# Kernel optimization log

Hardware: AMD Instinct MI355X
Metric: run time of the kernel (lower is better)

Reference implementation:

```python
import jax, jax.numpy as jnp
import numpy as np
from jax import lax

DN = ('NHWC', 'HWIO', 'NHWC')


def conv_same(x, w):
    return lax.conv_general_dilated(x, w, window_strides=(1, 1), padding='SAME',
                                    dimension_numbers=DN)


def dwconv(x, w):
    # w: (kh, kw, F, 1) TF depthwise layout -> HWIO (kh, kw, 1, F), groups=F
    F = w.shape[2]
    return lax.conv_general_dilated(x, jnp.transpose(w, (0, 1, 3, 2)),
                                    window_strides=(1, 1), padding='SAME',
                                    dimension_numbers=DN, feature_group_count=F)


def hard_sigmoid(x):
    return jnp.clip(0.2 * x + 0.5, 0.0, 1.0)


def setup_inputs() -> dict:
    key = jax.random.key(0)
    ks = jax.random.split(key, 10)
    B, H, W, Cin, F = 16, 128, 128, 64, 64
    s = 0.05
    return {
        'inputs': jax.random.normal(ks[0], (B, H, W, Cin), jnp.float32),
        'h0': jax.random.normal(ks[1], (B, H, W, F), jnp.float32),
        'c0': jax.random.normal(ks[2], (B, H, W, F), jnp.float32),
        'm0': jax.random.normal(ks[3], (B, H, W, F), jnp.float32),
        'kernel': jax.random.normal(ks[4], (3, 3, Cin, 4 * F), jnp.float32) * s,
        'recurrent_kernel': jax.random.normal(ks[5], (3, 3, F, 4 * F), jnp.float32) * s,
        'bias': jnp.concatenate([jnp.zeros((F,), jnp.float32),
                                 jnp.ones((F,), jnp.float32),
                                 jnp.zeros((2 * F,), jnp.float32)]),
        'sa_kernel': jax.random.normal(ks[6], (1, 1, F, 5), jnp.float32) * s,
        'kernel_z': jax.random.normal(ks[7], (3, 3, 2, F), jnp.float32) * s,
        'depth_wise_kernel': jax.random.normal(ks[8], (3, 3, F, 6), jnp.float32) * s,
        'sa_bias': jnp.zeros((3 * F,), jnp.float32),
    }


def reference(inputs, h0, c0, m0, kernel, recurrent_kernel, bias, sa_kernel,
              kernel_z, depth_wise_kernel, sa_bias):
    F = h0.shape[-1]
    # --- ConvLSTM gates (no dropout: all four gates share the same input, so
    # a single fused conv over the 4F-channel kernel is the same math) ---
    xz = conv_same(inputs, kernel) + bias  # [B,H,W,4F]
    hz = conv_same(h0, recurrent_kernel)   # [B,H,W,4F]
    z = xz + hz
    zi_, zf_, zc_, zo_ = jnp.split(z, 4, axis=-1)
    i = hard_sigmoid(zi_)
    f = hard_sigmoid(zf_)
    c = f * c0 + i * jnp.tanh(zc_)
    o = hard_sigmoid(zo_)
    h = o * jnp.tanh(c)  # [B,H,W,F]

    # --- Self-attention memory (SAM) module; 1x1 convs -> channel contractions ---
    w = sa_kernel[0, 0]  # [F,5]
    v_h = jnp.einsum('bhwc,c->bhw', h, w[:, 0])
    k_h = jnp.einsum('bhwc,c->bhw', h, w[:, 1])
    q_h = jnp.einsum('bhwc,c->bhw', h, w[:, 2])
    k_m = jnp.einsum('bhwc,c->bhw', m0, w[:, 3])
    v_m = jnp.einsum('bhwc,c->bhw', m0, w[:, 4])

    alpha_m = jax.nn.softmax(jnp.matmul(q_h, k_m), axis=-1)  # [B,H,H] (H==W)
    alpha_h = jax.nn.softmax(jnp.matmul(q_h, k_h), axis=-1)
    z_m = jnp.matmul(alpha_m, v_m)  # [B,H,W]
    z_h = jnp.matmul(alpha_h, v_h)

    zi = conv_same(jnp.stack([z_h, z_m], axis=-1), kernel_z)  # [B,H,W,F]

    dw = depth_wise_kernel  # [3,3,F,6]
    b_i, b_g, b_o = jnp.split(sa_bias, 3)
    i2 = jax.nn.sigmoid(dwconv(zi, dw[..., 0:1]) + dwconv(h, dw[..., 1:2]) + b_i)
    g = jnp.tanh(dwconv(zi, dw[..., 2:3]) + dwconv(h, dw[..., 3:4]) + b_g)
    o2 = jax.nn.sigmoid(dwconv(zi, dw[..., 4:5]) + dwconv(h, dw[..., 5:6]) + b_o)

    m_t = (1.0 - i2) * m0 + i2 * g
    h_hat = m_t * o2
    return h_hat, c, m_t
```

## Files before the change

### kernel.cpp

```cpp
#include <hip/hip_runtime.h>

#define BB 16
#define HH 128
#define WW 128
#define FF 64
#define NPIX (BB*HH*WW)

typedef short bf16x8 __attribute__((ext_vector_type(8)));
typedef float f32x4 __attribute__((ext_vector_type(4)));

__device__ __forceinline__ float bf2f(unsigned int u){ return __uint_as_float(u<<16); }
__device__ __forceinline__ unsigned short f2bf(float f){
  unsigned u = __float_as_uint(f);
  u += 0x7fffu + ((u>>16)&1u);
  return (unsigned short)(u>>16);
}
__device__ __forceinline__ float hsig(float x){ return fminf(fmaxf(fmaf(0.2f,x,0.5f),0.f),1.f); }
__device__ __forceinline__ float tanh_fast(float x){
  float e = __expf(2.f*x);
  return 1.f - 2.f/(e + 1.f);
}
__device__ __forceinline__ void gload_lds16(const void* g, void* l){
  __builtin_amdgcn_global_load_lds(
      (const __attribute__((address_space(1))) unsigned int*)g,
      (__attribute__((address_space(3))) unsigned int*)l, 16, 0, 0);
}

__global__ __launch_bounds__(256) void prep_all(
    const float* __restrict__ in, const float* __restrict__ h0,
    const float* __restrict__ kern, const float* __restrict__ rkern,
    unsigned short* __restrict__ Xp, unsigned short* __restrict__ Wg){
  const int blk = blockIdx.x;
  const int t = threadIdx.x;
  if (blk < 33){
    int i = blk*256 + t;
    if (i >= 16*516) return;
    int b = i / 516, r = i % 516;
    int y, x;
    if (r < 130){ y = 0; x = r; }
    else if (r < 260){ y = 129; x = r-130; }
    else if (r < 388){ y = r-260+1; x = 0; }
    else { y = r-388+1; x = 129; }
    unsigned short* p = Xp + (((size_t)(b*130 + y)*130) + x)*128;
    uint4 z = {0u,0u,0u,0u};
    #pragma unroll
    for (int c=0;c<16;++c) ((uint4*)p)[c] = z;
  } else if (blk < 33 + 16384){
    int gi = (blk-33)*256 + t;
    int pix = gi >> 4;
    int ch8 = (gi & 15) * 8;
    const float* src = (ch8 < 64) ? (in + (size_t)pix*64 + ch8)
                                  : (h0 + (size_t)pix*64 + (ch8-64));
    float4 v0 = *(const float4*)src;
    float4 v1 = *(const float4*)(src+4);
    uint4 o;
    o.x = (unsigned)f2bf(v0.x) | ((unsigned)f2bf(v0.y)<<16);
    o.y = (unsigned)f2bf(v0.z) | ((unsigned)f2bf(v0.w)<<16);
    o.z = (unsigned)f2bf(v1.x) | ((unsigned)f2bf(v1.y)<<16);
    o.w = (unsigned)f2bf(v1.z) | ((unsigned)f2bf(v1.w)<<16);
    int b = pix >> 14, y = (pix >> 7) & 127, x = pix & 127;
    *(uint4*)(Xp + (((size_t)(b*130 + y+1)*130) + (x+1))*128 + ch8) = o;
  } else {
    int k = blk - (33 + 16384);
    int n = t;
    int tap = k >> 7, c = k & 127;
    float v = (c < 64) ? kern[((size_t)(tap*64 + c))*256 + n]
                       : rkern[((size_t)(tap*64 + (c-64)))*256 + n];
    Wg[(size_t)n*1152 + k] = f2bf(v);
  }
}

__global__ __launch_bounds__(256, 2) void gates_kernel(
    const unsigned short* __restrict__ Xp,
    const unsigned short* __restrict__ Wg,
    const float* __restrict__ bias,
    const float* __restrict__ c0,
    float* __restrict__ c_out,
    unsigned short* __restrict__ h_bf){
  __shared__ unsigned short As[2][130*128];
  const int gid = blockIdx.x;
  const int swz = (gid & 7)*256 + (gid >> 3);
  const int b  = swz >> 7;
  const int y  = swz & 127;
  const int tid = threadIdx.x;
  const int l = tid & 63;
  const int wid = tid >> 6;
  const int l15 = l & 15, l4 = l >> 4;
  const int n0 = wid*16 + l15;

  const unsigned short* brow[4];
  #pragma unroll
  for (int g=0; g<4; ++g) brow[g] = Wg + (size_t)(g*64 + n0)*1152 + l4*8;

  f32x4 acc[8][4];
  #pragma unroll
  for (int mf=0;mf<8;++mf)
    #pragma unroll
    for (int g=0;g<4;++g) acc[mf][g] = (f32x4){0.f,0.f,0.f,0.f};

  auto stage = [&](int buf, int dyi){
    const unsigned short* gbase = Xp + ((size_t)((b*130 + y + dyi)*130))*128;
    unsigned short* lbase = &As[buf][0];
    #pragma unroll
    for (int it=0; it<8; ++it){
      int q = it*256 + tid;
      int px = q >> 4, c = q & 15;
      int cs = c ^ (px & 7);
      gload_lds16(gbase + (size_t)px*128 + cs*8, lbase + (size_t)q*8);
    }
    if (l < 8){
      int q = 2048 + wid*8 + l;
      int px = q >> 4, c = q & 15;
      int cs = c ^ (px & 7);
      gload_lds16(gbase + (size_t)px*128 + cs*8, lbase + (size_t)q*8);
    }
  };

  stage(0, 0);
  for (int dyi = 0; dyi < 3; ++dyi){
    if (dyi < 2){
      stage((dyi+1)&1, dyi+1);
      asm volatile("s_waitcnt vmcnt(9)" ::: "memory");
    } else {
      asm volatile("s_waitcnt vmcnt(0)" ::: "memory");
    }
    __builtin_amdgcn_sched_barrier(0);
    __builtin_amdgcn_s_barrier();
    __builtin_amdgcn_sched_barrier(0);
    const unsigned short* asb = &As[dyi&1][0];
    #pragma unroll
    for (int dxi = 0; dxi < 3; ++dxi){
      const int tap = dyi*3 + dxi;
      #pragma unroll
      for (int ksc = 0; ksc < 2; ++ksc){
        bf16x8 bfr[4][2];
        #pragma unroll
        for (int g=0; g<4; ++g)
          #pragma unroll
          for (int k2=0; k2<2; ++k2)
            bfr[g][k2] = *(const bf16x8*)(brow[g] + tap*128 + (ksc*2+k2)*32);
        #pragma unroll
        for (int k2=0; k2<2; ++k2){
          const int cd = (ksc*2+k2)*4 + l4;
          #pragma unroll
          for (int mf=0; mf<8; ++mf){
            const int px = mf*16 + l15 + dxi;
            bf16x8 a = *(const bf16x8*)(asb + (size_t)px*128 + ((cd ^ (px & 7))*8));
            #pragma unroll
            for (int g=0;g<4;++g)
              acc[mf][g] = __builtin_amdgcn_mfma_f32_16x16x32_bf16(a, bfr[g][k2], acc[mf][g], 0,0,0);
          }
        }
      }
    }
    __builtin_amdgcn_sched_barrier(0);
    __builtin_amdgcn_s_barrier();
    __builtin_amdgcn_sched_barrier(0);
  }
  const float b0 = bias[n0], b1 = bias[64+n0], b2 = bias[128+n0], b3 = bias[192+n0];
  const size_t prow = (size_t)(b*128 + y)*128;
  #pragma unroll
  for (int mf=0;mf<8;++mf){
    #pragma unroll
    for (int r=0;r<4;++r){
      const int x = mf*16 + l4*4 + r;
      const size_t p = prow + x;
      const float zi_ = acc[mf][0][r] + b0;
      const float zf_ = acc[mf][1][r] + b1;
      const float zc_ = acc[mf][2][r] + b2;
      const float zo_ = acc[mf][3][r] + b3;
      const float iv = hsig(zi_), fv = hsig(zf_), ov = hsig(zo_);
      const float cv = fv*c0[p*64 + n0] + iv*tanh_fast(zc_);
      const float hv = ov*tanh_fast(cv);
      c_out[p*64 + n0] = cv;
      h_bf[p*64 + n0] = f2bf(hv);
    }
  }
}

__global__ __launch_bounds__(256) void qkv_kernel(
    const unsigned short* __restrict__ h_bf, const float* __restrict__ m0,
    const float* __restrict__ sak,
    float* __restrict__ q_h, float* __restrict__ k_h, float* __restrict__ v_h,
    float* __restrict__ k_m, float* __restrict__ v_m){
  __shared__ float wS[320];
  for (int i = threadIdx.x; i < 320; i += 256) wS[i] = sak[i];
  __syncthreads();
  const int p = blockIdx.x*256 + threadIdx.x;
  const unsigned short* hp = h_bf + (size_t)p*64;
  const float* mp = m0 + (size_t)p*64;
  float a0=0,a1=0,a2=0,a3=0,a4=0;
  #pragma unroll
  for (int ch = 0; ch < 64; ch += 8){
    uint4 hu = *(const uint4*)(hp + ch);
    float4 ma = *(const float4*)(mp + ch);
    float4 mb = *(const float4*)(mp + ch + 4);
    float hv[8] = { bf2f(hu.x&0xffffu), bf2f(hu.x>>16), bf2f(hu.y&0xffffu), bf2f(hu.y>>16),
                    bf2f(hu.z&0xffffu), bf2f(hu.z>>16), bf2f(hu.w&0xffffu), bf2f(hu.w>>16) };
    float mv[8] = { ma.x,ma.y,ma.z,ma.w, mb.x,mb.y,mb.z,mb.w };
    #pragma unroll
    for (int jj=0;jj<8;++jj){
      const float* w = &wS[(ch+jj)*5];
      a0 = fmaf(hv[jj], w[0], a0);
      a1 = fmaf(hv[jj], w[1], a1);
      a2 = fmaf(hv[jj], w[2], a2);
      a3 = fmaf(mv[jj], w[3], a3);
      a4 = fmaf(mv[jj], w[4], a4);
    }
  }
  v_h[p]=a0; k_h[p]=a1; q_h[p]=a2; k_m[p]=a3; v_m[p]=a4;
}

__global__ __launch_bounds__(256) void attn_kernel(
    const float* __restrict__ q_h, const float* __restrict__ k_h, const float* __restrict__ v_h,
    const float* __restrict__ k_m, const float* __restrict__ v_m,
    float* __restrict__ z_h, float* __restrict__ z_m){
  __shared__ float Kl[128][132];
  __shared__ float Vl[128][132];
  __shared__ float q2[8][132];
  __shared__ float al[8][132];
  const int bid = blockIdx.x;
  const int b = bid >> 4;
  const int type = (bid >> 3) & 1;
  const int rb = bid & 7;
  const float* K = (type ? k_m : k_h) + (size_t)b*16384;
  const float* V = (type ? v_m : v_h) + (size_t)b*16384;
  const float* Q = q_h + (size_t)b*16384;
  float* Z = (type ? z_m : z_h) + (size_t)b*16384;
  const int t = threadIdx.x;
  const int jq = t & 31;
  const int r8 = t >> 5;

  for (int base = 0; base < 16384; base += 1024){
    const int idx = base + t*4;
    const int w = idx >> 7, j = idx & 127;
    const float4 kv = *(const float4*)(K + idx);
    const float4 vv = *(const float4*)(V + idx);
    *(float4*)&Kl[w][j] = kv;
    *(float4*)&Vl[w][j] = vv;
  }

  for (int p = 0; p < 2; ++p){
    __syncthreads();
    for (int idx = t; idx < 1024; idx += 256)
      q2[idx>>7][idx&127] = Q[(rb*16 + p*8 + (idx>>7))*128 + (idx&127)];
    __syncthreads();
    const int i = rb*16 + p*8 + r8;
    float s0=0.f,s1=0.f,s2=0.f,s3=0.f;
    #pragma unroll 8
    for (int w=0; w<128; ++w){
      const float qv = q2[r8][w];
      const float4 kv = *(const float4*)&Kl[w][jq*4];
      s0 = fmaf(qv, kv.x, s0); s1 = fmaf(qv, kv.y, s1);
      s2 = fmaf(qv, kv.z, s2); s3 = fmaf(qv, kv.w, s3);
    }
    float mx = fmaxf(fmaxf(s0,s1), fmaxf(s2,s3));
    #pragma unroll
    for (int o=1;o<32;o<<=1) mx = fmaxf(mx, __shfl_xor(mx, o));
    const float p0 = __expf(s0-mx), p1 = __expf(s1-mx);
    const float p2 = __expf(s2-mx), p3 = __expf(s3-mx);
    float sm = (p0+p1)+(p2+p3);
    #pragma unroll
    for (int o=1;o<32;o<<=1) sm += __shfl_xor(sm, o);
    const float inv = 1.f/sm;
    *(float4*)&al[r8][jq*4] = make_float4(p0*inv, p1*inv, p2*inv, p3*inv);
    __syncthreads();
    float z0=0.f,z1=0.f,z2=0.f,z3=0.f;
    #pragma unroll 8
    for (int w=0; w<128; ++w){
      const float av = al[r8][w];
      const float4 vv = *(const float4*)&Vl[w][jq*4];
      z0 = fmaf(av, vv.x, z0); z1 = fmaf(av, vv.y, z1);
      z2 = fmaf(av, vv.z, z2); z3 = fmaf(av, vv.w, z3);
    }
    *(float4*)(Z + (size_t)i*128 + jq*4) = make_float4(z0,z1,z2,z3);
  }
}

__global__ __launch_bounds__(512) void final_fused(
    const float* __restrict__ z_h, const float* __restrict__ z_m,
    const float* __restrict__ kz,
    const unsigned short* __restrict__ h_bf,
    const float* __restrict__ m0, const float* __restrict__ dwk,
    const float* __restrict__ sab,
    float* __restrict__ hhat, float* __restrict__ m_t){
  __shared__ unsigned short zi[4][128][64];
  const int f = threadIdx.x & 63;
  const int g = threadIdx.x >> 6;
  const int blk = blockIdx.x;
  const int b = blk >> 6;
  const int y0 = (blk & 63) * 2;

  {
    const int ry = g >> 1;
    const int xh = g & 1;
    const int yy = y0 - 1 + ry;
    const int x0 = xh * 64;
    if ((unsigned)yy >= 128u){
      for (int i=0;i<64;++i) zi[ry][x0+i][f] = 0;
    } else {
      float w0[9], w1[9];
      #pragma unroll
      for (int tap=0; tap<9; ++tap){
        w0[tap] = kz[tap*128 + f];
        w1[tap] = kz[tap*128 + 64 + f];
      }
      const float* zhr = z_h + (size_t)(b*128 + yy)*128;
      const float* zmr = z_m + (size_t)(b*128 + yy)*128;
      const bool ym = (yy > 0), yp = (yy < 127);
      float az[3][3], am[3][3];
      auto ldc = [&](int x, float (&Z)[3], float (&M)[3]){
        if ((unsigned)x < 128u){
          Z[0] = ym ? zhr[x-128] : 0.f;  M[0] = ym ? zmr[x-128] : 0.f;
          Z[1] = zhr[x];                 M[1] = zmr[x];
          Z[2] = yp ? zhr[x+128] : 0.f;  M[2] = yp ? zmr[x+128] : 0.f;
        } else { Z[0]=Z[1]=Z[2]=0.f; M[0]=M[1]=M[2]=0.f; }
      };
      ldc(x0-1, az[0], am[0]);
      ldc(x0,   az[1], am[1]);
      for (int i=0; i<64; ++i){
        const int x = x0 + i;
        ldc(x+1, az[2], am[2]);
        float acc = 0.f;
        #pragma unroll
        for (int tap=0; tap<9; ++tap){
          const int dy = tap/3, dx = tap%3;
          acc = fmaf(az[dx][dy], w0[tap], acc);
          acc = fmaf(am[dx][dy], w1[tap], acc);
        }
        zi[ry][x][f] = f2bf(acc);
        #pragma unroll
        for (int k=0;k<3;++k){
          az[0][k]=az[1][k]; az[1][k]=az[2][k];
          am[0][k]=am[1][k]; am[1][k]=am[2][k];
        }
      }
    }
  }
  __syncthreads();

  const int r2 = g >> 2;
  const int xq = g & 3;
  const int y = y0 + r2;
  const size_t rb = (size_t)(b*128 + y)*128;
  float wv[9][6];
  #pragma unroll
  for (int tap=0;tap<9;++tap)
    #pragma unroll
    for (int jj=0;jj<6;++jj) wv[tap][jj] = dwk[(tap*64 + f)*6 + jj];
  const float bi = sab[f], bg = sab[64+f], bo = sab[128+f];
  const bool ym = (y > 0), yp = (y < 127);
  float vz[3][3], vh[3][3];
  auto ldc2 = [&](int x, float (&Z)[3], float (&H)[3]){
    if ((unsigned)x < 128u){
      const size_t base = (rb + x)*64 + f;
      H[0] = ym ? bf2f(h_bf[base - 8192]) : 0.f;
      H[1] = bf2f(h_bf[base]);
      H[2] = yp ? bf2f(h_bf[base + 8192]) : 0.f;
      Z[0] = bf2f(zi[r2  ][x][f]);
      Z[1] = bf2f(zi[r2+1][x][f]);
      Z[2] = bf2f(zi[r2+2][x][f]);
    } else { Z[0]=Z[1]=Z[2]=0.f; H[0]=H[1]=H[2]=0.f; }
  };
  const int x0 = xq*32;
  ldc2(x0-1, vz[0], vh[0]);
  ldc2(x0,   vz[1], vh[1]);
  for (int i=0; i<32; ++i){
    const int x = x0 + i;
    ldc2(x+1, vz[2], vh[2]);
    float si=0.f, sg=0.f, so=0.f;
    #pragma unroll
    for (int tap=0;tap<9;++tap){
      const int dy = tap/3, dx = tap%3;
      const float zv = vz[dx][dy], hv = vh[dx][dy];
      si = fmaf(zv, wv[tap][0], si); si = fmaf(hv, wv[tap][1], si);
      sg = fmaf(zv, wv[tap][2], sg); sg = fmaf(hv, wv[tap][3], sg);
      so = fmaf(zv, wv[tap][4], so); so = fmaf(hv, wv[tap][5], so);
    }
    const size_t p = rb + x;
    const float i2 = 1.f/(1.f+__expf(-(si+bi)));
    const float gg = tanh_fast(sg+bg);
    const float o2 = 1.f/(1.f+__expf(-(so+bo)));
    const float mv = m0[p*64+f];
    const float mt = (1.f-i2)*mv + i2*gg;
    hhat[p*64+f] = mt*o2;
    m_t[p*64+f]  = mt;
    #pragma unroll
    for (int k=0;k<3;++k){
      vz[0][k]=vz[1][k]; vz[1][k]=vz[2][k];
      vh[0][k]=vh[1][k]; vh[1][k]=vh[2][k];
    }
  }
}

extern "C" void kernel_launch(void* const* d_in, const int* in_sizes, int n_in,
                              void* d_out, int out_size, void* d_ws, size_t ws_size,
                              hipStream_t stream){
  const float* inputs = (const float*)d_in[0];
  const float* h0p    = (const float*)d_in[1];
  const float* c0p    = (const float*)d_in[2];
  const float* m0p    = (const float*)d_in[3];
  const float* kern   = (const float*)d_in[4];
  const float* rkern  = (const float*)d_in[5];
  const float* biasp  = (const float*)d_in[6];
  const float* sakp   = (const float*)d_in[7];
  const float* kzp    = (const float*)d_in[8];
  const float* dwkp   = (const float*)d_in[9];
  const float* sabp   = (const float*)d_in[10];
  float* out = (float*)d_out;
  char* ws = (char*)d_ws;

  constexpr size_t SZ_XP  = (size_t)16*130*130*128*2;
  constexpr size_t SZ_WG  = (size_t)256*1152*2;
  constexpr size_t SZ_HBF = (size_t)NPIX*64*2;
  constexpr size_t SZA    = (size_t)NPIX*4;
  constexpr size_t OFF_XP  = 0;
  constexpr size_t OFF_WG  = OFF_XP + SZ_XP;
  constexpr size_t OFF_HBF = OFF_WG + SZ_WG;
  constexpr size_t OFF_Q   = OFF_HBF + SZ_HBF;
  constexpr size_t OFF_KH  = OFF_Q  + SZA;
  constexpr size_t OFF_VH  = OFF_KH + SZA;
  constexpr size_t OFF_KM  = OFF_VH + SZA;
  constexpr size_t OFF_VM  = OFF_KM + SZA;
  constexpr size_t OFF_ZH  = OFF_VM + SZA;
  constexpr size_t OFF_ZM  = OFF_ZH + SZA;

  unsigned short* Xp  = (unsigned short*)(ws + OFF_XP);
  unsigned short* Wg  = (unsigned short*)(ws + OFF_WG);
  unsigned short* Hbf = (unsigned short*)(ws + OFF_HBF);
  float* Qh = (float*)(ws + OFF_Q);
  float* Kh = (float*)(ws + OFF_KH);
  float* Vh = (float*)(ws + OFF_VH);
  float* Km = (float*)(ws + OFF_KM);
  float* Vm = (float*)(ws + OFF_VM);
  float* Zh = (float*)(ws + OFF_ZH);
  float* Zm = (float*)(ws + OFF_ZM);

  prep_all<<<33 + 16384 + 1152, 256, 0, stream>>>(inputs, h0p, kern, rkern, Xp, Wg);
  gates_kernel<<<2048, 256, 0, stream>>>(Xp, Wg, biasp, c0p,
                                         out + (size_t)NPIX*64, Hbf);
  qkv_kernel<<<NPIX/256, 256, 0, stream>>>(Hbf, m0p, sakp, Qh, Kh, Vh, Km, Vm);
  attn_kernel<<<256, 256, 0, stream>>>(Qh, Kh, Vh, Km, Vm, Zh, Zm);
  final_fused<<<1024, 512, 0, stream>>>(Zh, Zm, kzp, Hbf, m0p, dwkp, sabp,
                                        out, out + 2*(size_t)NPIX*64);
}
```

Measured before the change: 401.8 us.

## Restructure gates conv GEMM to two-row tiles with LDS-staged weights

The gates kernel now processes two output rows per 512-thread block and iterates over 18 K-slices (tap × 64-channel half). Each slice double-buffers both activations and a permuted weight tile into LDS through async global-to-LDS loads, rather than reading weights from global memory inside the MFMA loop. Weights are reordered in prep so each wave's gate columns are contiguous. The change also adds intra-slice barriers and s_setprio around the MFMA bursts. It trades the old per-row activation reuse across dx taps for more barriers and a larger per-slice LDS footprint.

```diff
diff --git a/kernel.cpp b/kernel.cpp
--- a/kernel.cpp
+++ b/kernel.cpp
@@ -62,35 +62,38 @@
     *(uint4*)(Xp + (((size_t)(b*130 + y+1)*130) + (x+1))*128 + ch8) = o;
   } else {
     int k = blk - (33 + 16384);
-    int n = t;
+    int np = t;
     int tap = k >> 7, c = k & 127;
+    int wid = np >> 6, r = np & 63;
+    int gate = r >> 4, ch16 = r & 15;
+    int n = gate*64 + wid*16 + ch16;
     float v = (c < 64) ? kern[((size_t)(tap*64 + c))*256 + n]
                        : rkern[((size_t)(tap*64 + (c-64)))*256 + n];
-    Wg[(size_t)n*1152 + k] = f2bf(v);
-  }
-}
-
-__global__ __launch_bounds__(256, 2) void gates_kernel(
+    Wg[(size_t)np*1152 + k] = f2bf(v);
+  }
+}
+
+__global__ __launch_bounds__(512, 1) void gates_kernel(
     const unsigned short* __restrict__ Xp,
     const unsigned short* __restrict__ Wg,
     const float* __restrict__ bias,
     const float* __restrict__ c0,
     float* __restrict__ c_out,
     unsigned short* __restrict__ h_bf){
-  __shared__ unsigned short As[2][130*128];
+  __shared__ unsigned short Ab[2][256*64];
+  __shared__ unsigned short Bb[2][256*64];
   const int gid = blockIdx.x;
-  const int swz = (gid & 7)*256 + (gid >> 3);
-  const int b  = swz >> 7;
-  const int y  = swz & 127;
+  const int swz = (gid & 7)*128 + (gid >> 3);
+  const int b  = swz >> 6;
+  const int y0 = (swz & 63)*2;
   const int tid = threadIdx.x;
   const int l = tid & 63;
-  const int wid = tid >> 6;
+  const int wv = tid >> 6;
+  const int wid = wv & 3;
+  const int mh  = wv >> 2;
   const int l15 = l & 15, l4 = l >> 4;
-  const int n0 = wid*16 + l15;
-
-  const unsigned short* brow[4];
-  #pragma unroll
-  for (int g=0; g<4; ++g) brow[g] = Wg + (size_t)(g*64 + n0)*1152 + l4*8;
+  const int e7  = l15 & 7;
+  const int n0  = wid*16 + l15;
 
   f32x4 acc[8][4];
   #pragma unroll
@@ -98,67 +101,78 @@
     #pragma unroll
     for (int g=0;g<4;++g) acc[mf][g] = (f32x4){0.f,0.f,0.f,0.f};
 
-  auto stage = [&](int buf, int dyi){
-    const unsigned short* gbase = Xp + ((size_t)((b*130 + y + dyi)*130))*128;
-    unsigned short* lbase = &As[buf][0];
-    #pragma unroll
-    for (int it=0; it<8; ++it){
-      int q = it*256 + tid;
-      int px = q >> 4, c = q & 15;
+  auto stage = [&](int buf, int ks){
+    const int tap = ks >> 1, ch0 = (ks & 1)*64;
+    const int dy = tap/3, dx = tap%3;
+    const unsigned short* ga =
+        Xp + ((size_t)((b*130 + y0 + dy)*130) + dx)*128 + ch0;
+    const unsigned short* gb = Wg + tap*128 + ch0;
+    unsigned short* la = &Ab[buf][0];
+    unsigned short* lb = &Bb[buf][0];
+    #pragma unroll
+    for (int i=0; i<4; ++i){
+      int q = i*512 + tid;
+      int px = q >> 3, c = q & 7;
       int cs = c ^ (px & 7);
-      gload_lds16(gbase + (size_t)px*128 + cs*8, lbase + (size_t)q*8);
-    }
-    if (l < 8){
-      int q = 2048 + wid*8 + l;
-      int px = q >> 4, c = q & 15;
-      int cs = c ^ (px & 7);
-      gload_lds16(gbase + (size_t)px*128 + cs*8, lbase + (size_t)q*8);
+      gload_lds16(ga + ((size_t)((px>>7)*130 + (px&127)))*128 + cs*8,
+                  la + (size_t)q*8);
+    }
+    #pragma unroll
+    for (int i=0; i<4; ++i){
+      int q = i*512 + tid;
+      int nr = q >> 3, c = q & 7;
+      int cs = c ^ (nr & 7);
+      gload_lds16(gb + (size_t)nr*1152 + cs*8,
+                  lb + (size_t)q*8);
     }
   };
 
   stage(0, 0);
-  for (int dyi = 0; dyi < 3; ++dyi){
-    if (dyi < 2){
-      stage((dyi+1)&1, dyi+1);
-      asm volatile("s_waitcnt vmcnt(9)" ::: "memory");
+  int cb = 0;
+  for (int ks = 0; ks < 18; ++ks){
+    if (ks < 17){
+      stage(cb^1, ks+1);
+      asm volatile("s_waitcnt vmcnt(8)" ::: "memory");
     } else {
       asm volatile("s_waitcnt vmcnt(0)" ::: "memory");
     }
     __builtin_amdgcn_sched_barrier(0);
     __builtin_amdgcn_s_barrier();
     __builtin_amdgcn_sched_barrier(0);
-    const unsigned short* asb = &As[dyi&1][0];
-    #pragma unroll
-    for (int dxi = 0; dxi < 3; ++dxi){
-      const int tap = dyi*3 + dxi;
+    const unsigned short* At = &Ab[cb][0];
+    const unsigned short* Bt = &Bb[cb][0];
+    #pragma unroll
+    for (int ph = 0; ph < 4; ++ph){
+      const int k2 = ph >> 1, mq = ph & 1;
+      const int ck = ((k2*4 + l4) ^ e7)*8;
+      bf16x8 bfr[4], af[4];
       #pragma unroll
-      for (int ksc = 0; ksc < 2; ++ksc){
-        bf16x8 bfr[4][2];
+      for (int g=0; g<4; ++g)
+        bfr[g] = *(const bf16x8*)(Bt + (size_t)(wid*64 + g*16 + l15)*64 + ck);
+      #pragma unroll
+      for (int m=0; m<4; ++m){
+        const int px = mh*128 + (mq*4 + m)*16 + l15;
+        af[m] = *(const bf16x8*)(At + (size_t)px*64 + ck);
+      }
+      __builtin_amdgcn_s_barrier();
+      asm volatile("s_waitcnt lgkmcnt(0)" ::: "memory");
+      __builtin_amdgcn_sched_barrier(0);
+      __builtin_amdgcn_s_setprio(1);
+      #pragma unroll
+      for (int m=0; m<4; ++m)
         #pragma unroll
         for (int g=0; g<4; ++g)
-          #pragma unroll
-          for (int k2=0; k2<2; ++k2)
-            bfr[g][k2] = *(const bf16x8*)(brow[g] + tap*128 + (ksc*2+k2)*32);
-        #pragma unroll
-        for (int k2=0; k2<2; ++k2){
-          const int cd = (ksc*2+k2)*4 + l4;
-          #pragma unroll
-          for (int mf=0; mf<8; ++mf){
-            const int px = mf*16 + l15 + dxi;
-            bf16x8 a = *(const bf16x8*)(asb + (size_t)px*128 + ((cd ^ (px & 7))*8));
-            #pragma unroll
-            for (int g=0;g<4;++g)
-              acc[mf][g] = __builtin_amdgcn_mfma_f32_16x16x32_bf16(a, bfr[g][k2], acc[mf][g], 0,0,0);
-          }
-        }
-      }
-    }
-    __builtin_amdgcn_sched_barrier(0);
-    __builtin_amdgcn_s_barrier();
-    __builtin_amdgcn_sched_barrier(0);
-  }
+          acc[mq*4+m][g] = __builtin_amdgcn_mfma_f32_16x16x32_bf16(
+                               af[m], bfr[g], acc[mq*4+m][g], 0,0,0);
+      __builtin_amdgcn_s_setprio(0);
+      __builtin_amdgcn_sched_barrier(0);
+      __builtin_amdgcn_s_barrier();
+    }
+    cb ^= 1;
+  }
+
   const float b0 = bias[n0], b1 = bias[64+n0], b2 = bias[128+n0], b3 = bias[192+n0];
-  const size_t prow = (size_t)(b*128 + y)*128;
+  const size_t prow = (size_t)(b*128 + y0 + mh)*128;
   #pragma unroll
   for (int mf=0;mf<8;++mf){
     #pragma unroll
@@ -437,7 +451,7 @@
   float* Zm = (float*)(ws + OFF_ZM);
 
   prep_all<<<33 + 16384 + 1152, 256, 0, stream>>>(inputs, h0p, kern, rkern, Xp, Wg);
-  gates_kernel<<<2048, 256, 0, stream>>>(Xp, Wg, biasp, c0p,
+  gates_kernel<<<1024, 512, 0, stream>>>(Xp, Wg, biasp, c0p,
                                          out + (size_t)NPIX*64, Hbf);
   qkv_kernel<<<NPIX/256, 256, 0, stream>>>(Hbf, m0p, sakp, Qh, Kh, Vh, Km, Vm);
   attn_kernel<<<256, 256, 0, stream>>>(Qh, Kh, Vh, Km, Vm, Zh, Zm);
```

Result: slower. 422.5 us (+5.2%).
